# Performance work log

Measured on AMD Instinct MI355X. Metric: run time of the kernel, lower is better.

The kernel has to match this reference:

```python
import jax, jax.numpy as jnp
import numpy as np

SIZE = 1024
HEADS = 16
HEAD_SIZE = SIZE // HEADS
B, S = 2, 2048


def setup_inputs() -> dict:
    key = jax.random.key(0)
    ks = jax.random.split(key, 12)
    def lin(kw, kb, fan_in, fan_out):
        # mimic nn.Linear default init U(-1/sqrt(fan_in), 1/sqrt(fan_in))
        bound = 1.0 / np.sqrt(fan_in)
        W = jax.random.uniform(kw, (fan_out, fan_in), jnp.float32, -bound, bound)
        b = jax.random.uniform(kb, (fan_out,), jnp.float32, -bound, bound)
        return W, b
    Wk, bk = lin(ks[0], ks[1], SIZE, SIZE)
    Wv, bv = lin(ks[2], ks[3], SIZE, SIZE)
    Wq, bq = lin(ks[4], ks[5], SIZE, SIZE)
    Wo, bo = lin(ks[6], ks[7], SIZE, SIZE)
    k_in = jax.random.normal(ks[8], (B, S, SIZE), jnp.float32)
    v_in = jax.random.normal(ks[9], (B, S, SIZE), jnp.float32)
    q_in = jax.random.normal(ks[10], (B, S, SIZE), jnp.float32)
    # causal mask: True = masked out (as in torch masked_fill_)
    mask = jnp.triu(jnp.ones((S, S), dtype=bool), k=1)
    return {"key": k_in, "value": v_in, "query": q_in, "mask": mask,
            "Wk": Wk, "bk": bk, "Wv": Wv, "bv": bv,
            "Wq": Wq, "bq": bq, "Wo": Wo, "bo": bo}


def _shape(x):
    # [B, S, size] -> [B, H, S, head_size]
    b, s, _ = x.shape
    return x.reshape(b, s, HEADS, HEAD_SIZE).transpose(0, 2, 1, 3)


def reference(key, value, query, mask, Wk, bk, Wv, bv, Wq, bq, Wo, bo):
    k = _shape(key @ Wk.T + bk)      # [B,H,S,D]
    v = _shape(value @ Wv.T + bv)
    q = _shape(query @ Wq.T + bq)
    scale = jnp.sqrt(jnp.float32(HEAD_SIZE))
    scores = jnp.einsum('bhqd,bhkd->bhqk', q, k) / scale
    scores = jnp.where(mask, -jnp.inf, scores)
    attn = jax.nn.softmax(scores, axis=-1)
    out = jnp.einsum('bhqk,bhkd->bhqd', attn, v)  # [B,H,S,D]
    out = out.transpose(0, 2, 1, 3).reshape(out.shape[0], out.shape[2], SIZE)
    out = out @ Wo.T + bo
    return out, attn
```

## Files before the change

kernel.cpp:

```cpp
#include <hip/hip_runtime.h>
#include <stdint.h>

typedef unsigned short u16_t;
typedef unsigned int   u32_t;
using short8 = __attribute__((ext_vector_type(8))) short;
using f32x4  = __attribute__((ext_vector_type(4))) float;
using u32x4  = __attribute__((ext_vector_type(4))) unsigned int;

#define SEQ   2048
#define SZ    1024
#define NH    16
#define DH    64
#define NBH   32
#define MTOK  4096

#define GPTR(p) ((__attribute__((address_space(1))) void*)(uintptr_t)(p))
#define LPTR(p) ((__attribute__((address_space(3))) void*)(p))

__device__ __forceinline__ u16_t f2bf(float f) {
  union { float f; u32_t i; } v; v.f = f;
  return (u16_t)((v.i + 0x7FFFu + ((v.i >> 16) & 1u)) >> 16);
}

union pk8 { u16_t u[8]; uint4 v; };
__device__ __forceinline__ uint4 cvt8(const float* src) {
  pk8 p;
  #pragma unroll
  for (int i = 0; i < 8; i++) p.u[i] = f2bf(src[i]);
  return p.v;
}

struct CvtArgs { const float* s[7]; u16_t* d[7]; int n[7]; };

__global__ __launch_bounds__(256) void cvt_bf16(CvtArgs a) {
  const int seg = blockIdx.y;
  const float* __restrict__ src = a.s[seg];
  u16_t* __restrict__ dst = a.d[seg];
  const int n8 = a.n[seg] >> 3;
  for (int i = blockIdx.x * 256 + threadIdx.x; i < n8; i += gridDim.x * 256) {
    float f[8];
    *(float4*)&f[0] = ((const float4*)src)[(size_t)i * 2];
    *(float4*)&f[4] = ((const float4*)src)[(size_t)i * 2 + 1];
    ((uint4*)dst)[i] = cvt8(f);
  }
}

struct QkvArgs {
  const u16_t* A[3]; const u16_t* W[3]; const float* bias[3]; u16_t* out[3];
};

__global__ __launch_bounds__(256) void gemm_qkv(QkvArgs ga)
{
  __shared__ __align__(16) u16_t sA[128 * 32];
  __shared__ __align__(16) u16_t sB[128 * 32];
  const int z = blockIdx.z;
  const u16_t* __restrict__ A    = ga.A[z];
  const u16_t* __restrict__ W    = ga.W[z];
  const float* __restrict__ bias = ga.bias[z];
  u16_t* __restrict__ C          = ga.out[z];
  const int K = SZ;
  const int t = threadIdx.x;
  const int w = t >> 6, lane = t & 63, q = lane >> 4, l16 = lane & 15;
  const int wm = (w >> 1) * 64, wn = (w & 1) * 64;
  const int m0 = blockIdx.y * 128, n0 = blockIdx.x * 128;
  const int r0 = t >> 2;
  const int c0 = (t & 3) * 8;
  const u16_t* Ap = &A[(size_t)(m0 + r0) * K + c0];
  const u16_t* Bp = &W[(size_t)(n0 + r0) * K + c0];

  f32x4 acc[4][4] = {};

  for (int kb = 0; kb < K; kb += 32) {
    __builtin_amdgcn_global_load_lds(GPTR(Ap + kb),                  LPTR(&sA[t * 8]),        16, 0, 0);
    __builtin_amdgcn_global_load_lds(GPTR(Ap + (size_t)64 * K + kb), LPTR(&sA[2048 + t * 8]), 16, 0, 0);
    __builtin_amdgcn_global_load_lds(GPTR(Bp + kb),                  LPTR(&sB[t * 8]),        16, 0, 0);
    __builtin_amdgcn_global_load_lds(GPTR(Bp + (size_t)64 * K + kb), LPTR(&sB[2048 + t * 8]), 16, 0, 0);
    __syncthreads();
    short8 af[4], bf[4];
    #pragma unroll
    for (int i = 0; i < 4; i++) {
      af[i] = *(const short8*)&sA[(wm + i * 16 + l16) * 32 + q * 8];
      bf[i] = *(const short8*)&sB[(wn + i * 16 + l16) * 32 + q * 8];
    }
    #pragma unroll
    for (int mi = 0; mi < 4; mi++)
      #pragma unroll
      for (int ni = 0; ni < 4; ni++)
        acc[mi][ni] = __builtin_amdgcn_mfma_f32_16x16x32_bf16(af[mi], bf[ni], acc[mi][ni], 0, 0, 0);
    __syncthreads();
  }

  #pragma unroll
  for (int ni = 0; ni < 4; ni++) {
    const int cg = n0 + wn + ni * 16 + l16;
    const float bv = bias[cg];
    #pragma unroll
    for (int mi = 0; mi < 4; mi++) {
      const int rg0 = m0 + wm + mi * 16 + q * 4;
      if (z < 2) {
        #pragma unroll
        for (int r = 0; r < 4; r++)
          C[(size_t)(rg0 + r) * SZ + cg] = f2bf(acc[mi][ni][r] + bv);
      } else {
        const int trow = ((rg0 >> 11) * NH + (cg >> 6)) * DH + (cg & (DH - 1));
        const int s0 = rg0 & (SEQ - 1);
        union { u16_t u[4]; uint2 v; } pk;
        #pragma unroll
        for (int r = 0; r < 4; r++) pk.u[r] = f2bf(acc[mi][ni][r] + bv);
        *(uint2*)&C[(size_t)trow * SEQ + s0] = pk.v;
      }
    }
  }
}

__global__ __launch_bounds__(256) void gemm_bt(
    const u16_t* __restrict__ A, const u16_t* __restrict__ W,
    const float* __restrict__ bias, float* __restrict__ C,
    const int M, const int N, const int K)
{
  __shared__ __align__(16) u16_t sA[128 * 32];
  __shared__ __align__(16) u16_t sB[64 * 32];
  const int t = threadIdx.x;
  const int w = t >> 6, lane = t & 63, q = lane >> 4, l16 = lane & 15;
  const int wm = (w >> 1) * 64, wn = (w & 1) * 32;
  const int m0 = blockIdx.y * 128, n0 = blockIdx.x * 64;
  const int r0 = t >> 2;
  const int c0 = (t & 3) * 8;
  const u16_t* Ap = &A[(size_t)(m0 + r0) * K + c0];
  const u16_t* Bp = &W[(size_t)(n0 + r0) * K + c0];

  f32x4 acc[4][2] = {};

  for (int kb = 0; kb < K; kb += 32) {
    __builtin_amdgcn_global_load_lds(GPTR(Ap + kb),                  LPTR(&sA[t * 8]),        16, 0, 0);
    __builtin_amdgcn_global_load_lds(GPTR(Ap + (size_t)64 * K + kb), LPTR(&sA[2048 + t * 8]), 16, 0, 0);
    __builtin_amdgcn_global_load_lds(GPTR(Bp + kb),                  LPTR(&sB[t * 8]),        16, 0, 0);
    __syncthreads();
    short8 af[4], bf[2];
    #pragma unroll
    for (int i = 0; i < 4; i++)
      af[i] = *(const short8*)&sA[(wm + i * 16 + l16) * 32 + q * 8];
    #pragma unroll
    for (int j = 0; j < 2; j++)
      bf[j] = *(const short8*)&sB[(wn + j * 16 + l16) * 32 + q * 8];
    #pragma unroll
    for (int mi = 0; mi < 4; mi++)
      #pragma unroll
      for (int ni = 0; ni < 2; ni++)
        acc[mi][ni] = __builtin_amdgcn_mfma_f32_16x16x32_bf16(af[mi], bf[ni], acc[mi][ni], 0, 0, 0);
    __syncthreads();
  }

  #pragma unroll
  for (int ni = 0; ni < 2; ni++) {
    const int cg = n0 + wn + ni * 16 + l16;
    const float bv = bias[cg];
    #pragma unroll
    for (int mi = 0; mi < 4; mi++) {
      const int rg0 = m0 + wm + mi * 16 + q * 4;
      #pragma unroll
      for (int r = 0; r < 4; r++)
        C[(size_t)(rg0 + r) * N + cg] = acc[mi][ni][r] + bv;
    }
  }
}

__global__ __launch_bounds__(256, 4) void attn_fused(
    const u16_t* __restrict__ Qp, const u16_t* __restrict__ Kp,
    const u16_t* __restrict__ VT, float* __restrict__ attn,
    u16_t* __restrict__ AO)
{
  __shared__ __align__(16) u16_t Pbuf[4][16 * 32];
  const int t = threadIdx.x;
  const int w = t >> 6, lane = t & 63, q = lane >> 4, l16 = lane & 15;
  const int bh = blockIdx.x, b = bh >> 4;
  const int h = bh & (NH - 1);
  float* attn_bh = attn + (size_t)bh * SEQ * SEQ;

  const int y = 31 - (int)blockIdx.y;
  const int i0 = y * 64;
  const int wrow0 = i0 + w * 16;
  const size_t qbase = ((size_t)(b * SEQ + wrow0 + l16)) * SZ + h * DH + q * 8;
  const short8 qf0 = *(const short8*)&Qp[qbase];
  const short8 qf1 = *(const short8*)&Qp[qbase + 32];
  const int tmax = (i0 >> 4) + w;
  const int njt  = (i0 >> 4) + 4;

  float l[4] = {0.f, 0.f, 0.f, 0.f};
  #pragma unroll 2
  for (int jt = 0; jt <= tmax; jt++) {
    const int j0 = jt * 16;
    const size_t kbase = ((size_t)(b * SEQ + j0 + l16)) * SZ + h * DH + q * 8;
    const short8 kf0 = *(const short8*)&Kp[kbase];
    const short8 kf1 = *(const short8*)&Kp[kbase + 32];
    f32x4 s = {};
    s = __builtin_amdgcn_mfma_f32_16x16x32_bf16(qf0, kf0, s, 0, 0, 0);
    s = __builtin_amdgcn_mfma_f32_16x16x32_bf16(qf1, kf1, s, 0, 0, 0);
    #pragma unroll
    for (int r = 0; r < 4; r++) {
      const int row = wrow0 + q * 4 + r;
      const int col = j0 + l16;
      l[r] += (col <= row) ? __expf(s[r] * 0.125f) : 0.0f;
    }
  }
  float rl[4];
  #pragma unroll
  for (int r = 0; r < 4; r++) {
    float ps = l[r];
    ps += __shfl_xor(ps, 1);
    ps += __shfl_xor(ps, 2);
    ps += __shfl_xor(ps, 4);
    ps += __shfl_xor(ps, 8);
    rl[r] = 1.0f / ps;
  }

  {
    const int zc0 = (y + 1) * 64;
    const int nz4 = (SEQ - zc0) >> 2;
    const u32x4 z = {0u, 0u, 0u, 0u};
    for (int r = 0; r < 16; r++) {
      u32x4* d4 = (u32x4*)(attn_bh + (size_t)(wrow0 + r) * SEQ + zc0);
      for (int c = lane; c < nz4; c += 64)
        __builtin_nontemporal_store(z, d4 + c);
    }
  }

  f32x4 o[4] = {};
  for (int pr = 0; pr < njt / 2; pr++) {
    const int t0 = pr * 2;
    if (t0 > tmax) {
      #pragma unroll
      for (int uu = 0; uu < 2; uu++) {
        const int j0 = (t0 + uu) * 16;
        #pragma unroll
        for (int r = 0; r < 4; r++)
          __builtin_nontemporal_store(
              0.0f, &attn_bh[(size_t)(wrow0 + q * 4 + r) * SEQ + j0 + l16]);
      }
      continue;
    }
    #pragma unroll
    for (int uu = 0; uu < 2; uu++) {
      const int jt = t0 + uu, j0 = jt * 16;
      const size_t kbase = ((size_t)(b * SEQ + j0 + l16)) * SZ + h * DH + q * 8;
      const short8 kf0 = *(const short8*)&Kp[kbase];
      const short8 kf1 = *(const short8*)&Kp[kbase + 32];
      f32x4 s = {};
      s = __builtin_amdgcn_mfma_f32_16x16x32_bf16(qf0, kf0, s, 0, 0, 0);
      s = __builtin_amdgcn_mfma_f32_16x16x32_bf16(qf1, kf1, s, 0, 0, 0);
      #pragma unroll
      for (int r = 0; r < 4; r++) {
        const int row = wrow0 + q * 4 + r;
        const int col = j0 + l16;
        const float p = (col <= row) ? __expf(s[r] * 0.125f) * rl[r] : 0.0f;
        __builtin_nontemporal_store(p, &attn_bh[(size_t)row * SEQ + col]);
        Pbuf[w][(q * 4 + r) * 32 + uu * 16 + l16] = f2bf(p);
      }
    }
    __asm__ volatile("s_waitcnt lgkmcnt(0)" ::: "memory");
    const short8 pf = *(const short8*)&Pbuf[w][l16 * 32 + q * 8];
    #pragma unroll
    for (int n = 0; n < 4; n++) {
      const size_t vbase = ((size_t)(bh * DH + n * 16 + l16)) * SEQ + t0 * 16 + q * 8;
      const short8 vf = *(const short8*)&VT[vbase];
      o[n] = __builtin_amdgcn_mfma_f32_16x16x32_bf16(pf, vf, o[n], 0, 0, 0);
    }
  }

  #pragma unroll
  for (int n = 0; n < 4; n++)
    #pragma unroll
    for (int r = 0; r < 4; r++)
      AO[(size_t)(b * SEQ + wrow0 + q * 4 + r) * SZ + h * DH + n * 16 + l16] = f2bf(o[n][r]);
}

extern "C" void kernel_launch(void* const* d_in, const int* in_sizes, int n_in,
                              void* d_out, int out_size, void* d_ws, size_t ws_size,
                              hipStream_t stream) {
  const float* key   = (const float*)d_in[0];
  const float* value = (const float*)d_in[1];
  const float* query = (const float*)d_in[2];
  const float* Wk = (const float*)d_in[4];
  const float* bk = (const float*)d_in[5];
  const float* Wv = (const float*)d_in[6];
  const float* bv = (const float*)d_in[7];
  const float* Wq = (const float*)d_in[8];
  const float* bq = (const float*)d_in[9];
  const float* Wo = (const float*)d_in[10];
  const float* bo = (const float*)d_in[11];

  float* out  = (float*)d_out;
  float* attn = out + (size_t)MTOK * SZ;

  u16_t* Qp  = (u16_t*)d_ws;
  u16_t* Kp  = Qp  + (size_t)MTOK * SZ;
  u16_t* VTv = Kp  + (size_t)MTOK * SZ;
  u16_t* AO  = VTv + (size_t)MTOK * SZ;
  u16_t* Qb  = AO  + (size_t)MTOK * SZ;
  u16_t* Kb  = Qb  + (size_t)MTOK * SZ;
  u16_t* Vb  = Kb  + (size_t)MTOK * SZ;
  u16_t* Wqb = Vb  + (size_t)MTOK * SZ;
  u16_t* Wkb = Wqb + (size_t)SZ * SZ;
  u16_t* Wvb = Wkb + (size_t)SZ * SZ;
  u16_t* Wob = Wvb + (size_t)SZ * SZ;

  CvtArgs ca;
  ca.s[0] = query; ca.d[0] = Qb;  ca.n[0] = MTOK * SZ;
  ca.s[1] = key;   ca.d[1] = Kb;  ca.n[1] = MTOK * SZ;
  ca.s[2] = value; ca.d[2] = Vb;  ca.n[2] = MTOK * SZ;
  ca.s[3] = Wq;    ca.d[3] = Wqb; ca.n[3] = SZ * SZ;
  ca.s[4] = Wk;    ca.d[4] = Wkb; ca.n[4] = SZ * SZ;
  ca.s[5] = Wv;    ca.d[5] = Wvb; ca.n[5] = SZ * SZ;
  ca.s[6] = Wo;    ca.d[6] = Wob; ca.n[6] = SZ * SZ;
  cvt_bf16<<<dim3(256, 7), 256, 0, stream>>>(ca);

  QkvArgs ga;
  ga.A[0] = Qb;  ga.W[0] = Wqb; ga.bias[0] = bq; ga.out[0] = Qp;
  ga.A[1] = Kb;  ga.W[1] = Wkb; ga.bias[1] = bk; ga.out[1] = Kp;
  ga.A[2] = Vb;  ga.W[2] = Wvb; ga.bias[2] = bv; ga.out[2] = VTv;
  gemm_qkv<<<dim3(SZ / 128, MTOK / 128, 3), 256, 0, stream>>>(ga);

  attn_fused<<<dim3(NBH, 32), 256, 0, stream>>>(Qp, Kp, VTv, attn, AO);

  gemm_bt<<<dim3(SZ / 64, MTOK / 128), 256, 0, stream>>>(AO, Wob, bo, out, MTOK, SZ, SZ);
}
```

Before: 817.7 us.

## Remap blocks across XCDs and prefetch K/V loads in attention kernel

Remaps the linear block index in both GEMMs and the attention kernel so that tiles sharing the same rows or the same batch-head land on the same XCD, aiming to improve L2 reuse. In the attention kernel, the sum pass now software-prefetches the next K tile while the current one is computed. The output pass hoists all K and V loads ahead of the MFMAs. MFMA sections are wrapped in s_setprio, and the occupancy hint of 4 is dropped from launch_bounds. The added registers may lower occupancy, and the remap assumes round-robin dispatch of blocks across XCDs.

```diff
diff --git a/kernel.cpp b/kernel.cpp
--- a/kernel.cpp
+++ b/kernel.cpp
@@ -62,7 +62,10 @@
   const int t = threadIdx.x;
   const int w = t >> 6, lane = t & 63, q = lane >> 4, l16 = lane & 15;
   const int wm = (w >> 1) * 64, wn = (w & 1) * 64;
-  const int m0 = blockIdx.y * 128, n0 = blockIdx.x * 128;
+  const int dlin = blockIdx.x + 8 * blockIdx.y;
+  const int xcd = dlin & 7, jj = dlin >> 3;
+  const int m0 = (xcd * 4 + (jj >> 3)) * 128;
+  const int n0 = (jj & 7) * 128;
   const int r0 = t >> 2;
   const int c0 = (t & 3) * 8;
   const u16_t* Ap = &A[(size_t)(m0 + r0) * K + c0];
@@ -123,7 +126,10 @@
   const int t = threadIdx.x;
   const int w = t >> 6, lane = t & 63, q = lane >> 4, l16 = lane & 15;
   const int wm = (w >> 1) * 64, wn = (w & 1) * 32;
-  const int m0 = blockIdx.y * 128, n0 = blockIdx.x * 64;
+  const int dlin = blockIdx.x + 16 * blockIdx.y;
+  const int xcd = dlin & 7, jj = dlin >> 3;
+  const int m0 = (xcd * 4 + (jj >> 4)) * 128;
+  const int n0 = (jj & 15) * 64;
   const int r0 = t >> 2;
   const int c0 = (t & 3) * 8;
   const u16_t* Ap = &A[(size_t)(m0 + r0) * K + c0];
@@ -165,7 +171,7 @@
   }
 }
 
-__global__ __launch_bounds__(256, 4) void attn_fused(
+__global__ __launch_bounds__(256) void attn_fused(
     const u16_t* __restrict__ Qp, const u16_t* __restrict__ Kp,
     const u16_t* __restrict__ VT, float* __restrict__ attn,
     u16_t* __restrict__ AO)
@@ -173,11 +179,14 @@
   __shared__ __align__(16) u16_t Pbuf[4][16 * 32];
   const int t = threadIdx.x;
   const int w = t >> 6, lane = t & 63, q = lane >> 4, l16 = lane & 15;
-  const int bh = blockIdx.x, b = bh >> 4;
+  const int dlin = blockIdx.x + NBH * blockIdx.y;
+  const int xcd = dlin & 7, jj = dlin >> 3;
+  const int bh = xcd * 4 + (jj & 3);
+  const int y  = 31 - (jj >> 2);
+  const int b = bh >> 4;
   const int h = bh & (NH - 1);
   float* attn_bh = attn + (size_t)bh * SEQ * SEQ;
 
-  const int y = 31 - (int)blockIdx.y;
   const int i0 = y * 64;
   const int wrow0 = i0 + w * 16;
   const size_t qbase = ((size_t)(b * SEQ + wrow0 + l16)) * SZ + h * DH + q * 8;
@@ -186,22 +195,29 @@
   const int tmax = (i0 >> 4) + w;
   const int njt  = (i0 >> 4) + 4;
 
+  const size_t krow = (size_t)(b * SEQ + l16) * SZ + h * DH + q * 8;
+
   float l[4] = {0.f, 0.f, 0.f, 0.f};
-  #pragma unroll 2
+  short8 kc0 = *(const short8*)&Kp[krow];
+  short8 kc1 = *(const short8*)&Kp[krow + 32];
   for (int jt = 0; jt <= tmax; jt++) {
+    const int jn = (jt < tmax) ? jt + 1 : tmax;
+    const size_t kn = krow + (size_t)jn * 16 * SZ;
+    const short8 nf0 = *(const short8*)&Kp[kn];
+    const short8 nf1 = *(const short8*)&Kp[kn + 32];
+    f32x4 s = {};
+    __builtin_amdgcn_s_setprio(1);
+    s = __builtin_amdgcn_mfma_f32_16x16x32_bf16(qf0, kc0, s, 0, 0, 0);
+    s = __builtin_amdgcn_mfma_f32_16x16x32_bf16(qf1, kc1, s, 0, 0, 0);
+    __builtin_amdgcn_s_setprio(0);
     const int j0 = jt * 16;
-    const size_t kbase = ((size_t)(b * SEQ + j0 + l16)) * SZ + h * DH + q * 8;
-    const short8 kf0 = *(const short8*)&Kp[kbase];
-    const short8 kf1 = *(const short8*)&Kp[kbase + 32];
-    f32x4 s = {};
-    s = __builtin_amdgcn_mfma_f32_16x16x32_bf16(qf0, kf0, s, 0, 0, 0);
-    s = __builtin_amdgcn_mfma_f32_16x16x32_bf16(qf1, kf1, s, 0, 0, 0);
     #pragma unroll
     for (int r = 0; r < 4; r++) {
       const int row = wrow0 + q * 4 + r;
       const int col = j0 + l16;
       l[r] += (col <= row) ? __expf(s[r] * 0.125f) : 0.0f;
     }
+    kc0 = nf0; kc1 = nf1;
   }
   float rl[4];
   #pragma unroll
@@ -239,32 +255,43 @@
       }
       continue;
     }
-    #pragma unroll
-    for (int uu = 0; uu < 2; uu++) {
-      const int jt = t0 + uu, j0 = jt * 16;
-      const size_t kbase = ((size_t)(b * SEQ + j0 + l16)) * SZ + h * DH + q * 8;
-      const short8 kf0 = *(const short8*)&Kp[kbase];
-      const short8 kf1 = *(const short8*)&Kp[kbase + 32];
-      f32x4 s = {};
-      s = __builtin_amdgcn_mfma_f32_16x16x32_bf16(qf0, kf0, s, 0, 0, 0);
-      s = __builtin_amdgcn_mfma_f32_16x16x32_bf16(qf1, kf1, s, 0, 0, 0);
-      #pragma unroll
-      for (int r = 0; r < 4; r++) {
-        const int row = wrow0 + q * 4 + r;
-        const int col = j0 + l16;
-        const float p = (col <= row) ? __expf(s[r] * 0.125f) * rl[r] : 0.0f;
-        __builtin_nontemporal_store(p, &attn_bh[(size_t)row * SEQ + col]);
-        Pbuf[w][(q * 4 + r) * 32 + uu * 16 + l16] = f2bf(p);
-      }
+    const size_t kb0 = krow + (size_t)t0 * 16 * SZ;
+    const short8 ka0 = *(const short8*)&Kp[kb0];
+    const short8 ka1 = *(const short8*)&Kp[kb0 + 32];
+    const short8 kb0v = *(const short8*)&Kp[kb0 + (size_t)16 * SZ];
+    const short8 kb1v = *(const short8*)&Kp[kb0 + (size_t)16 * SZ + 32];
+    short8 vf[4];
+    #pragma unroll
+    for (int n = 0; n < 4; n++)
+      vf[n] = *(const short8*)&VT[((size_t)(bh * DH + n * 16 + l16)) * SEQ + t0 * 16 + q * 8];
+
+    f32x4 s0 = {}, s1 = {};
+    __builtin_amdgcn_s_setprio(1);
+    s0 = __builtin_amdgcn_mfma_f32_16x16x32_bf16(qf0, ka0, s0, 0, 0, 0);
+    s0 = __builtin_amdgcn_mfma_f32_16x16x32_bf16(qf1, ka1, s0, 0, 0, 0);
+    s1 = __builtin_amdgcn_mfma_f32_16x16x32_bf16(qf0, kb0v, s1, 0, 0, 0);
+    s1 = __builtin_amdgcn_mfma_f32_16x16x32_bf16(qf1, kb1v, s1, 0, 0, 0);
+    __builtin_amdgcn_s_setprio(0);
+
+    #pragma unroll
+    for (int r = 0; r < 4; r++) {
+      const int row = wrow0 + q * 4 + r;
+      const int col0 = t0 * 16 + l16;
+      const float p0 = (col0 <= row) ? __expf(s0[r] * 0.125f) * rl[r] : 0.0f;
+      __builtin_nontemporal_store(p0, &attn_bh[(size_t)row * SEQ + col0]);
+      Pbuf[w][(q * 4 + r) * 32 + l16] = f2bf(p0);
+      const int col1 = col0 + 16;
+      const float p1 = (col1 <= row) ? __expf(s1[r] * 0.125f) * rl[r] : 0.0f;
+      __builtin_nontemporal_store(p1, &attn_bh[(size_t)row * SEQ + col1]);
+      Pbuf[w][(q * 4 + r) * 32 + 16 + l16] = f2bf(p1);
     }
     __asm__ volatile("s_waitcnt lgkmcnt(0)" ::: "memory");
     const short8 pf = *(const short8*)&Pbuf[w][l16 * 32 + q * 8];
-    #pragma unroll
-    for (int n = 0; n < 4; n++) {
-      const size_t vbase = ((size_t)(bh * DH + n * 16 + l16)) * SEQ + t0 * 16 + q * 8;
-      const short8 vf = *(const short8*)&VT[vbase];
-      o[n] = __builtin_amdgcn_mfma_f32_16x16x32_bf16(pf, vf, o[n], 0, 0, 0);
-    }
+    __builtin_amdgcn_s_setprio(1);
+    #pragma unroll
+    for (int n = 0; n < 4; n++)
+      o[n] = __builtin_amdgcn_mfma_f32_16x16x32_bf16(pf, vf[n], o[n], 0, 0, 0);
+    __builtin_amdgcn_s_setprio(0);
   }
 
   #pragma unroll
```

Result: no change. 816.7 us (-0.1%).
